# Kernel tuning notes

Hardware: AMD Instinct MI355X
Metric: run time of the kernel (lower is better)

Reference implementation:

```python
import jax, jax.numpy as jnp
import numpy as np

B, WAY, SHOT = 100, 5, 5            # B = way*shot + n_query = 25 + 75
C1, C2, D = 512, 640, 5             # F_L channels, F1 channels, disturb_num
S_L, S1 = 21, 42                    # F_L spatial, F1 spatial (square)
N = C2 * D                          # MLP width = 3200
WEIGHT = 0.5
EPS = 1e-5
GN_GROUPS = 16


def _dwconv1d(x, w):
    # x: (B, C, L), w: (C, 1, 7) depthwise, pad 3, no bias
    return jax.lax.conv_general_dilated(
        x, w, window_strides=(1,), padding=[(3, 3)],
        dimension_numbers=('NCH', 'OIH', 'NCH'),
        feature_group_count=x.shape[1])


def _group_norm(x, gamma, beta):
    # x: (B, C, L); GroupNorm(16, C), eps=1e-5
    b, c, l = x.shape
    xg = x.reshape(b, GN_GROUPS, -1)
    m = xg.mean(-1, keepdims=True)
    v = xg.var(-1, keepdims=True)
    xn = ((xg - m) * jax.lax.rsqrt(v + EPS)).reshape(b, c, l)
    return xn * gamma[None, :, None] + beta[None, :, None]


def setup_inputs() -> dict:
    key = jax.random.key(0)
    ks = jax.random.split(key, 8)
    inp = {
        'F1': jax.random.normal(ks[0], (B, C2, S1, S1), jnp.float32),
        'F_L': jax.random.normal(ks[1], (B, C1, S_L, S_L), jnp.float32),
        # structure_capture: depthwise Conv1d(C1, C1, 7, groups=C1, bias=False) + GroupNorm(16, C1)
        'sc_w': jax.random.normal(ks[2], (C1, 1, 7), jnp.float32) * 0.05,
        'gn_g': jnp.ones((C1,), jnp.float32),
        'gn_b': jnp.zeros((C1,), jnp.float32),
        # mask_branch: Conv2d(C1,16,1)+BN2d(16)+ReLU+Conv2d(16,D,1)
        'mb1_w': jax.random.normal(ks[3], (16, C1), jnp.float32) * 0.02,
        'mb1_b': jnp.zeros((16,), jnp.float32),
        'bn_g': jnp.ones((16,), jnp.float32),
        'bn_b': jnp.zeros((16,), jnp.float32),
        'mb2_w': jax.random.normal(ks[4], (D, 16), jnp.float32) * 0.02,
        'mb2_b': jnp.zeros((D,), jnp.float32),
        # both_mlp1 (resnet=True): BN1d(N) + Linear(N, N) + ELU
        'bn1d_g': jnp.ones((N,), jnp.float32),
        'bn1d_b': jnp.zeros((N,), jnp.float32),
        'lin_w': jax.random.normal(ks[5], (N, N), jnp.float32) * 0.01,
        'lin_b': jnp.zeros((N,), jnp.float32),
        'way': WAY,
        'shot': SHOT,
    }
    return inp


def _forward(F1, F_L, sc_w, gn_g, gn_b, mb1_w, mb1_b, bn_g, bn_b,
             mb2_w, mb2_b, bn1d_g, bn1d_b, lin_w, lin_b, way, shot):
    b = F_L.shape[0]
    # ---- structure_capture ----
    def gate(z):  # z: (B, C1, L)
        return jax.nn.sigmoid(_group_norm(_dwconv1d(z, sc_w), gn_g, gn_b))
    x_h = gate(F_L.mean(axis=3))[:, :, :, None]   # (B,C1,H,1)
    x_w = gate(F_L.mean(axis=2))[:, :, None, :]   # (B,C1,1,W)
    FLs = F_L * x_h * x_w

    # ---- bilinear upsample to F1 spatial (align_corners=False) ----
    s1 = F1.shape[-1]
    hm = jax.image.resize(FLs, (b, FLs.shape[1], s1, s1), method='bilinear')

    # ---- mask_branch (BatchNorm in eval mode: running_mean=0, running_var=1) ----
    h = jnp.einsum('bchw,oc->bohw', hm, mb1_w) + mb1_b[None, :, None, None]
    h = h * (bn_g * jax.lax.rsqrt(jnp.asarray(1.0 + EPS, h.dtype)))[None, :, None, None] \
        + bn_b[None, :, None, None]
    h = jax.nn.relu(h)
    heat = jnp.einsum('bchw,oc->bohw', h, mb2_w) + mb2_b[None, :, None, None]
    mask = jax.nn.sigmoid(heat)                   # (B, D, S1, S1)

    # ---- integration: fused weighted pooling (avoids (B,C2,D,HW) intermediate) ----
    f1 = F1.reshape(b, F1.shape[1], -1)           # (B, C2, HW)
    mk = mask.reshape(b, mask.shape[1], -1)       # (B, D, HW)
    sow = mk.sum(-1) + 1e-5                       # (B, D)
    vec = jnp.einsum('bcp,bdp->bcd', f1, mk) / sow[:, None, :]
    vec = vec.reshape(b, -1)                      # (B, C2*D)

    # ---- both_mlp1 (BN1d eval) + residual mix ----
    inv = jax.lax.rsqrt(jnp.asarray(1.0 + EPS, vec.dtype))
    z = vec * (bn1d_g * inv)[None, :] + bn1d_b[None, :]
    z = jax.nn.elu(z @ lin_w.T + lin_b[None, :])
    out = (1.0 - WEIGHT) * z + WEIGHT * vec

    support = out[:way * shot].reshape(way, shot, -1).mean(1)
    query = out[way * shot:]
    return support, query


def reference(F1, F_L, sc_w, gn_g, gn_b, mb1_w, mb1_b, bn_g, bn_b,
              mb2_w, mb2_b, bn1d_g, bn1d_b, lin_w, lin_b, way, shot):
    return _forward(F1, F_L, sc_w, gn_g, gn_b, mb1_w, mb1_b, bn_g, bn_b,
                    mb2_w, mb2_b, bn1d_g, bn1d_b, lin_w, lin_b, way, shot)
```

## Files before the change

kernel.cpp:

```cpp
#include <hip/hip_runtime.h>
#include <cstddef>

#define TPB 256

__device__ __forceinline__ float sigmoidf_(float x) {
  return 1.0f / (1.0f + __expf(-x));
}

__device__ __forceinline__ void rzmap(int i, int& j0, int& j1, float& w0, float& w1) {
  if (i == 0)            { j0 = 0;  j1 = 0;  w0 = 1.0f;  w1 = 0.0f; }
  else if (i == 41)      { j0 = 20; j1 = 20; w0 = 1.0f;  w1 = 0.0f; }
  else if ((i & 1) == 0) { int k = i >> 1; j0 = k - 1; j1 = k;     w0 = 0.25f; w1 = 0.75f; }
  else                   { int k = i >> 1; j0 = k;     j1 = k + 1; w0 = 0.75f; w1 = 0.25f; }
}

__global__ __launch_bounds__(256) void k1_gate_proj(
    const float* __restrict__ FL, const float* __restrict__ scw,
    const float* __restrict__ gng, const float* __restrict__ gnb,
    const float* __restrict__ mb1w, float* __restrict__ plc_part) {
  const int g = blockIdx.x, b = blockIdx.y;
  const int tid = threadIdx.x;
  __shared__ __align__(16) float slab[32 * 441];
  __shared__ float rm[672], cm[672], ch[672], cw[672];
  __shared__ float red[16];

  const float* base = FL + ((size_t)b * 512 + g * 32) * 441;
  const float4* b4 = (const float4*)base;
  float4* sl4 = (float4*)slab;
  for (int i = tid; i < 3528; i += TPB) sl4[i] = b4[i];
  __syncthreads();

  for (int idx = tid; idx < 672; idx += TPB) {
    int c = idx / 21, l = idx - c * 21;
    const float* rowp = slab + c * 441 + l * 21;
    float sr = 0.0f;
    #pragma unroll
    for (int w = 0; w < 21; ++w) sr += rowp[w];
    rm[idx] = sr * (1.0f / 21.0f);
    const float* colp = slab + c * 441 + l;
    float sc = 0.0f;
    #pragma unroll
    for (int h = 0; h < 21; ++h) sc += colp[h * 21];
    cm[idx] = sc * (1.0f / 21.0f);
  }
  __syncthreads();

  for (int idx = tid; idx < 672; idx += TPB) {
    int c = idx / 21, l = idx - c * 21;
    const float* w7 = scw + (g * 32 + c) * 7;
    float ah = 0.0f, aw = 0.0f;
    #pragma unroll
    for (int t = 0; t < 7; ++t) {
      int ll = l + t - 3;
      if (ll >= 0 && ll < 21) {
        float wt = w7[t];
        ah += rm[c * 21 + ll] * wt;
        aw += cm[c * 21 + ll] * wt;
      }
    }
    ch[idx] = ah; cw[idx] = aw;
  }
  __syncthreads();

  float s1 = 0.0f, s2 = 0.0f, s3 = 0.0f, s4v = 0.0f;
  for (int idx = tid; idx < 672; idx += TPB) {
    float x = ch[idx], y = cw[idx];
    s1 += x; s2 += x * x; s3 += y; s4v += y * y;
  }
  #pragma unroll
  for (int off = 32; off; off >>= 1) {
    s1 += __shfl_down(s1, off); s2 += __shfl_down(s2, off);
    s3 += __shfl_down(s3, off); s4v += __shfl_down(s4v, off);
  }
  if ((tid & 63) == 0) {
    int wv = tid >> 6;
    red[wv * 4 + 0] = s1; red[wv * 4 + 1] = s2;
    red[wv * 4 + 2] = s3; red[wv * 4 + 3] = s4v;
  }
  __syncthreads();
  const float S1 = red[0] + red[4] + red[8] + red[12];
  const float S2 = red[1] + red[5] + red[9] + red[13];
  const float S3 = red[2] + red[6] + red[10] + red[14];
  const float S4 = red[3] + red[7] + red[11] + red[15];
  const float invn = 1.0f / 672.0f;
  const float mh = S1 * invn, vh = S2 * invn - mh * mh;
  const float mw = S3 * invn, vw = S4 * invn - mw * mw;
  const float ivh = rsqrtf(vh + 1e-5f), ivw = rsqrtf(vw + 1e-5f);

  for (int idx = tid; idx < 672; idx += TPB) {
    int c = idx / 21;
    float gamma = gng[g * 32 + c], beta = gnb[g * 32 + c];
    ch[idx] = sigmoidf_((ch[idx] - mh) * ivh * gamma + beta);
    cw[idx] = sigmoidf_((cw[idx] - mw) * ivw * gamma + beta);
  }
  __syncthreads();

  float* pp = plc_part + ((size_t)g * 100 + b) * 7056;
  for (int p = tid; p < 441; p += TPB) {
    int i = p / 21, j = p - i * 21;
    float acc[16];
    #pragma unroll
    for (int o = 0; o < 16; ++o) acc[o] = 0.0f;
    #pragma unroll 4
    for (int c = 0; c < 32; ++c) {
      float v = slab[c * 441 + p] * ch[c * 21 + i] * cw[c * 21 + j];
      const float* wc = mb1w + g * 32 + c;
      #pragma unroll
      for (int o = 0; o < 16; ++o) acc[o] += v * wc[o * 512];
    }
    #pragma unroll
    for (int o = 0; o < 16; ++o) pp[(size_t)o * 441 + p] = acc[o];
  }
}

__global__ __launch_bounds__(256) void k1c_red(
    const float* __restrict__ pp, float* __restrict__ plc) {
  int i = blockIdx.x * TPB + threadIdx.x;
  if (i >= 705600) return;
  float s = 0.0f;
  #pragma unroll
  for (int g = 0; g < 16; ++g) s += pp[(size_t)g * 705600 + i];
  plc[i] = s;
}

__global__ __launch_bounds__(256) void k2_mask(
    const float* __restrict__ plc, const float* __restrict__ mb1b,
    const float* __restrict__ bng, const float* __restrict__ bnb,
    const float* __restrict__ mb2w, const float* __restrict__ mb2b,
    float* __restrict__ mask, float* __restrict__ sow) {
  const int b = blockIdx.x;
  const int p = blockIdx.y * TPB + threadIdx.x;
  float macc[5] = {0, 0, 0, 0, 0};
  if (p < 1764) {
    int y = p / 42, x = p - y * 42;
    int jy0, jy1, jx0, jx1; float wy0, wy1, wx0, wx1;
    rzmap(y, jy0, jy1, wy0, wy1);
    rzmap(x, jx0, jx1, wx0, wx1);
    const float RSQ = rsqrtf(1.0f + 1e-5f);
    const float* pb = plc + (size_t)b * 16 * 441;
    float h[16];
    #pragma unroll
    for (int o = 0; o < 16; ++o) {
      const float* po = pb + o * 441;
      float hm = wy0 * (wx0 * po[jy0 * 21 + jx0] + wx1 * po[jy0 * 21 + jx1]) +
                 wy1 * (wx0 * po[jy1 * 21 + jx0] + wx1 * po[jy1 * 21 + jx1]);
      float t = (hm + mb1b[o]) * (bng[o] * RSQ) + bnb[o];
      h[o] = t > 0.0f ? t : 0.0f;
    }
    #pragma unroll
    for (int d = 0; d < 5; ++d) {
      float acc = mb2b[d];
      #pragma unroll
      for (int o = 0; o < 16; ++o) acc += mb2w[d * 16 + o] * h[o];
      float mv = sigmoidf_(acc);
      mask[((size_t)b * 5 + d) * 1764 + p] = mv;
      macc[d] = mv;
    }
  }
  #pragma unroll
  for (int off = 32; off; off >>= 1) {
    #pragma unroll
    for (int d = 0; d < 5; ++d) macc[d] += __shfl_down(macc[d], off);
  }
  if ((threadIdx.x & 63) == 0) {
    #pragma unroll
    for (int d = 0; d < 5; ++d) atomicAdd(&sow[b * 5 + d], macc[d]);
  }
}

__global__ __launch_bounds__(256) void k3_vec(
    const float* __restrict__ F1, const float* __restrict__ mask,
    const float* __restrict__ sow, const float* __restrict__ g1d,
    float* __restrict__ vec_pad, float* __restrict__ vec_r) {
  const int ct = blockIdx.x, b = blockIdx.y;
  const int wv = threadIdx.x >> 6, lane = threadIdx.x & 63;
  const int c0 = ct * 16 + wv * 4;
  const float4* f0 = (const float4*)(F1 + ((size_t)b * 640 + c0) * 1764);
  const float4* mk = (const float4*)(mask + (size_t)b * 8820);
  float a[4][5] = {};
  for (int q = lane; q < 441; q += 64) {
    float4 f[4];
    #pragma unroll
    for (int j = 0; j < 4; ++j) f[j] = f0[(size_t)j * 441 + q];
    #pragma unroll
    for (int d = 0; d < 5; ++d) {
      float4 m = mk[d * 441 + q];
      #pragma unroll
      for (int j = 0; j < 4; ++j)
        a[j][d] += f[j].x * m.x + f[j].y * m.y + f[j].z * m.z + f[j].w * m.w;
    }
  }
  #pragma unroll
  for (int off = 32; off; off >>= 1) {
    #pragma unroll
    for (int j = 0; j < 4; ++j)
      #pragma unroll
      for (int d = 0; d < 5; ++d)
        a[j][d] += __shfl_down(a[j][d], off);
  }
  if (lane == 0) {
    const float RSQ = rsqrtf(1.0f + 1e-5f);
    #pragma unroll
    for (int j = 0; j < 4; ++j) {
      #pragma unroll
      for (int d = 0; d < 5; ++d) {
        float inv = 1.0f / (sow[b * 5 + d] + 1e-5f);
        float val = a[j][d] * inv;
        int k = (c0 + j) * 5 + d;
        vec_r[(size_t)b * 3200 + k] = val;
        vec_pad[(size_t)b * 3200 + k] = val * (g1d[k] * RSQ);
      }
    }
  }
}

__global__ __launch_bounds__(512) void k4_gemm(
    const float* __restrict__ A, const float* __restrict__ b1d,
    const float* __restrict__ W, float* __restrict__ dacc) {
  const int n0 = blockIdx.x * 64, ks = blockIdx.z;
  const int tid = threadIdx.x;
  const int tx = tid & 15, ty = tid >> 4;
  const int lr = tid >> 3, lq = tid & 7;
  __shared__ float4 As[8 * 132];
  __shared__ float4 Ws[8 * 68];
  const float4* A4 = (const float4*)A;
  const float4* B4 = (const float4*)b1d;
  const float4* W4 = (const float4*)W;
  const int kbase = ks * 80;
  const int r1 = lr + 64;
  float acc[4][4] = {};
  for (int kk = 0; kk < 10; ++kk) {
    __syncthreads();
    const int col = kbase + kk * 8 + lq;
    As[lq * 132 + lr] = A4[(size_t)lr * 800 + col];
    float4 va1;
    if (r1 < 100)       va1 = A4[(size_t)r1 * 800 + col];
    else if (r1 == 100) va1 = B4[col];
    else                va1 = make_float4(0.f, 0.f, 0.f, 0.f);
    As[lq * 132 + r1] = va1;
    Ws[lq * 68 + lr] = W4[(size_t)(n0 + lr) * 800 + col];
    __syncthreads();
    #pragma unroll
    for (int kq = 0; kq < 8; ++kq) {
      float4 av[4], bv[4];
      #pragma unroll
      for (int r = 0; r < 4; ++r) av[r] = As[kq * 132 + ty + 32 * r];
      #pragma unroll
      for (int s = 0; s < 4; ++s) bv[s] = Ws[kq * 68 + tx + 16 * s];
      #pragma unroll
      for (int r = 0; r < 4; ++r)
        #pragma unroll
        for (int s = 0; s < 4; ++s)
          acc[r][s] += av[r].x * bv[s].x + av[r].y * bv[s].y +
                       av[r].z * bv[s].z + av[r].w * bv[s].w;
    }
  }
  float* dp = dacc + (size_t)ks * 409600;
  #pragma unroll
  for (int r = 0; r < 4; ++r) {
    const int m = ty + 32 * r;
    #pragma unroll
    for (int s = 0; s < 4; ++s)
      dp[(size_t)m * 3200 + n0 + tx + 16 * s] = acc[r][s];
  }
}

__global__ __launch_bounds__(256) void k4b_epi(
    const float* __restrict__ dacc, const float* __restrict__ linb,
    const float* __restrict__ vec_r, float* __restrict__ out) {
  int i = blockIdx.x * TPB + threadIdx.x;
  if (i >= 320000) return;
  int m = i / 3200, n = i - m * 3200;
  const size_t S = 409600;
  size_t o = (size_t)m * 3200 + n;
  size_t oc = (size_t)100 * 3200 + n;
  float d = 0.0f, c0 = 0.0f;
  #pragma unroll
  for (int t = 0; t < 10; ++t) { d += dacc[t * S + o]; c0 += dacc[t * S + oc]; }
  float dv = d + c0 + linb[n];
  float z = dv > 0.0f ? dv : expm1f(dv);
  float ov = 0.5f * z + 0.5f * vec_r[i];
  if (m < 25) atomicAdd(out + (size_t)(m / 5) * 3200 + n, 0.2f * ov);
  else        out[(size_t)(m - 20) * 3200 + n] = ov;
}

extern "C" void kernel_launch(void* const* d_in, const int* in_sizes, int n_in,
                              void* d_out, int out_size, void* d_ws, size_t ws_size,
                              hipStream_t stream) {
  const float* F1   = (const float*)d_in[0];
  const float* FL   = (const float*)d_in[1];
  const float* scw  = (const float*)d_in[2];
  const float* gng  = (const float*)d_in[3];
  const float* gnb  = (const float*)d_in[4];
  const float* mb1w = (const float*)d_in[5];
  const float* mb1b = (const float*)d_in[6];
  const float* bng  = (const float*)d_in[7];
  const float* bnb  = (const float*)d_in[8];
  const float* mb2w = (const float*)d_in[9];
  const float* mb2b = (const float*)d_in[10];
  const float* g1d  = (const float*)d_in[11];
  const float* b1d  = (const float*)d_in[12];
  const float* linw = (const float*)d_in[13];
  const float* linb = (const float*)d_in[14];

  float* ws       = (float*)d_ws;
  float* plc      = ws;
  float* plc_part = ws + 705600;
  float* sow      = ws + 11995200;
  float* mask     = ws + 11995712;
  float* vec_pad  = ws + 12877712;
  float* vec_r    = ws + 13197712;
  float* dacc     = ws + 13517712;
  float* out      = (float*)d_out;

  hipMemsetAsync(sow, 0, 512 * sizeof(float), stream);
  hipMemsetAsync(out, 0, 16000 * sizeof(float), stream);
  k1_gate_proj<<<dim3(16, 100), TPB, 0, stream>>>(FL, scw, gng, gnb, mb1w, plc_part);
  k1c_red<<<dim3(2757), TPB, 0, stream>>>(plc_part, plc);
  k2_mask<<<dim3(100, 7), TPB, 0, stream>>>(plc, mb1b, bng, bnb, mb2w, mb2b, mask, sow);
  k3_vec<<<dim3(40, 100), TPB, 0, stream>>>(F1, mask, sow, g1d, vec_pad, vec_r);
  k4_gemm<<<dim3(50, 1, 10), 512, 0, stream>>>(vec_pad, b1d, linw, dacc);
  k4b_epi<<<dim3(1250), TPB, 0, stream>>>(dacc, linb, vec_r, out);
}
```

Before: 840.9 us.

## Halve gate-proj partials, recompute mask sums in k3, fold memsets into gemm

New measurement: 827.4 us. About the same (-1.6%).

```diff
diff --git a/kernel.cpp b/kernel.cpp
--- a/kernel.cpp
+++ b/kernel.cpp
@@ -18,98 +18,116 @@
     const float* __restrict__ FL, const float* __restrict__ scw,
     const float* __restrict__ gng, const float* __restrict__ gnb,
     const float* __restrict__ mb1w, float* __restrict__ plc_part) {
-  const int g = blockIdx.x, b = blockIdx.y;
+  const int gp = blockIdx.x, b = blockIdx.y;
   const int tid = threadIdx.x;
   __shared__ __align__(16) float slab[32 * 441];
   __shared__ float rm[672], cm[672], ch[672], cw[672];
   __shared__ float red[16];
 
-  const float* base = FL + ((size_t)b * 512 + g * 32) * 441;
-  const float4* b4 = (const float4*)base;
-  float4* sl4 = (float4*)slab;
-  for (int i = tid; i < 3528; i += TPB) sl4[i] = b4[i];
-  __syncthreads();
-
-  for (int idx = tid; idx < 672; idx += TPB) {
-    int c = idx / 21, l = idx - c * 21;
-    const float* rowp = slab + c * 441 + l * 21;
-    float sr = 0.0f;
-    #pragma unroll
-    for (int w = 0; w < 21; ++w) sr += rowp[w];
-    rm[idx] = sr * (1.0f / 21.0f);
-    const float* colp = slab + c * 441 + l;
-    float sc = 0.0f;
-    #pragma unroll
-    for (int h = 0; h < 21; ++h) sc += colp[h * 21];
-    cm[idx] = sc * (1.0f / 21.0f);
-  }
-  __syncthreads();
-
-  for (int idx = tid; idx < 672; idx += TPB) {
-    int c = idx / 21, l = idx - c * 21;
-    const float* w7 = scw + (g * 32 + c) * 7;
-    float ah = 0.0f, aw = 0.0f;
-    #pragma unroll
-    for (int t = 0; t < 7; ++t) {
-      int ll = l + t - 3;
-      if (ll >= 0 && ll < 21) {
-        float wt = w7[t];
-        ah += rm[c * 21 + ll] * wt;
-        aw += cm[c * 21 + ll] * wt;
+  const int p0 = tid;
+  const int p1 = tid + 256;
+  const int i0 = p0 / 21, j0 = p0 - i0 * 21;
+  const int i1 = p1 / 21, j1 = p1 - i1 * 21;
+  float acc0[16] = {}, acc1[16] = {};
+
+  for (int gi = 0; gi < 2; ++gi) {
+    const int g = gp * 2 + gi;
+    __syncthreads();
+
+    const float4* b4 = (const float4*)(FL + ((size_t)b * 512 + g * 32) * 441);
+    float4* sl4 = (float4*)slab;
+    for (int i = tid; i < 3528; i += TPB) sl4[i] = b4[i];
+    __syncthreads();
+
+    for (int idx = tid; idx < 672; idx += TPB) {
+      int c = idx / 21, l = idx - c * 21;
+      const float* rowp = slab + c * 441 + l * 21;
+      float sr = 0.0f;
+      #pragma unroll
+      for (int w = 0; w < 21; ++w) sr += rowp[w];
+      rm[idx] = sr * (1.0f / 21.0f);
+      const float* colp = slab + c * 441 + l;
+      float sc = 0.0f;
+      #pragma unroll
+      for (int h = 0; h < 21; ++h) sc += colp[h * 21];
+      cm[idx] = sc * (1.0f / 21.0f);
+    }
+    __syncthreads();
+
+    for (int idx = tid; idx < 672; idx += TPB) {
+      int c = idx / 21, l = idx - c * 21;
+      const float* w7 = scw + (g * 32 + c) * 7;
+      float ah = 0.0f, aw = 0.0f;
+      #pragma unroll
+      for (int t = 0; t < 7; ++t) {
+        int ll = l + t - 3;
+        if (ll >= 0 && ll < 21) {
+          float wt = w7[t];
+          ah += rm[c * 21 + ll] * wt;
+          aw += cm[c * 21 + ll] * wt;
+        }
       }
-    }
-    ch[idx] = ah; cw[idx] = aw;
-  }
-  __syncthreads();
-
-  float s1 = 0.0f, s2 = 0.0f, s3 = 0.0f, s4v = 0.0f;
-  for (int idx = tid; idx < 672; idx += TPB) {
-    float x = ch[idx], y = cw[idx];
-    s1 += x; s2 += x * x; s3 += y; s4v += y * y;
-  }
-  #pragma unroll
-  for (int off = 32; off; off >>= 1) {
-    s1 += __shfl_down(s1, off); s2 += __shfl_down(s2, off);
-    s3 += __shfl_down(s3, off); s4v += __shfl_down(s4v, off);
-  }
-  if ((tid & 63) == 0) {
-    int wv = tid >> 6;
-    red[wv * 4 + 0] = s1; red[wv * 4 + 1] = s2;
-    red[wv * 4 + 2] = s3; red[wv * 4 + 3] = s4v;
-  }
-  __syncthreads();
-  const float S1 = red[0] + red[4] + red[8] + red[12];
-  const float S2 = red[1] + red[5] + red[9] + red[13];
-  const float S3 = red[2] + red[6] + red[10] + red[14];
-  const float S4 = red[3] + red[7] + red[11] + red[15];
-  const float invn = 1.0f / 672.0f;
-  const float mh = S1 * invn, vh = S2 * invn - mh * mh;
-  const float mw = S3 * invn, vw = S4 * invn - mw * mw;
-  const float ivh = rsqrtf(vh + 1e-5f), ivw = rsqrtf(vw + 1e-5f);
-
-  for (int idx = tid; idx < 672; idx += TPB) {
-    int c = idx / 21;
-    float gamma = gng[g * 32 + c], beta = gnb[g * 32 + c];
-    ch[idx] = sigmoidf_((ch[idx] - mh) * ivh * gamma + beta);
-    cw[idx] = sigmoidf_((cw[idx] - mw) * ivw * gamma + beta);
-  }
-  __syncthreads();
-
-  float* pp = plc_part + ((size_t)g * 100 + b) * 7056;
-  for (int p = tid; p < 441; p += TPB) {
-    int i = p / 21, j = p - i * 21;
-    float acc[16];
-    #pragma unroll
-    for (int o = 0; o < 16; ++o) acc[o] = 0.0f;
+      ch[idx] = ah; cw[idx] = aw;
+    }
+    __syncthreads();
+
+    float s1 = 0.0f, s2 = 0.0f, s3 = 0.0f, s4v = 0.0f;
+    for (int idx = tid; idx < 672; idx += TPB) {
+      float x = ch[idx], y = cw[idx];
+      s1 += x; s2 += x * x; s3 += y; s4v += y * y;
+    }
+    #pragma unroll
+    for (int off = 32; off; off >>= 1) {
+      s1 += __shfl_down(s1, off); s2 += __shfl_down(s2, off);
+      s3 += __shfl_down(s3, off); s4v += __shfl_down(s4v, off);
+    }
+    if ((tid & 63) == 0) {
+      int wv = tid >> 6;
+      red[wv * 4 + 0] = s1; red[wv * 4 + 1] = s2;
+      red[wv * 4 + 2] = s3; red[wv * 4 + 3] = s4v;
+    }
+    __syncthreads();
+    const float S1 = red[0] + red[4] + red[8] + red[12];
+    const float S2 = red[1] + red[5] + red[9] + red[13];
+    const float S3 = red[2] + red[6] + red[10] + red[14];
+    const float S4 = red[3] + red[7] + red[11] + red[15];
+    const float invn = 1.0f / 672.0f;
+    const float mh = S1 * invn, vh = S2 * invn - mh * mh;
+    const float mw = S3 * invn, vw = S4 * invn - mw * mw;
+    const float ivh = rsqrtf(vh + 1e-5f), ivw = rsqrtf(vw + 1e-5f);
+
+    for (int idx = tid; idx < 672; idx += TPB) {
+      int c = idx / 21;
+      float gamma = gng[g * 32 + c], beta = gnb[g * 32 + c];
+      ch[idx] = sigmoidf_((ch[idx] - mh) * ivh * gamma + beta);
+      cw[idx] = sigmoidf_((cw[idx] - mw) * ivw * gamma + beta);
+    }
+    __syncthreads();
+
     #pragma unroll 4
     for (int c = 0; c < 32; ++c) {
-      float v = slab[c * 441 + p] * ch[c * 21 + i] * cw[c * 21 + j];
+      float v = slab[c * 441 + p0] * ch[c * 21 + i0] * cw[c * 21 + j0];
       const float* wc = mb1w + g * 32 + c;
       #pragma unroll
-      for (int o = 0; o < 16; ++o) acc[o] += v * wc[o * 512];
-    }
-    #pragma unroll
-    for (int o = 0; o < 16; ++o) pp[(size_t)o * 441 + p] = acc[o];
+      for (int o = 0; o < 16; ++o) acc0[o] += v * wc[o * 512];
+    }
+    if (p1 < 441) {
+      #pragma unroll 4
+      for (int c = 0; c < 32; ++c) {
+        float v = slab[c * 441 + p1] * ch[c * 21 + i1] * cw[c * 21 + j1];
+        const float* wc = mb1w + g * 32 + c;
+        #pragma unroll
+        for (int o = 0; o < 16; ++o) acc1[o] += v * wc[o * 512];
+      }
+    }
+  }
+
+  float* pp = plc_part + ((size_t)gp * 100 + b) * 7056;
+  #pragma unroll
+  for (int o = 0; o < 16; ++o) pp[(size_t)o * 441 + p0] = acc0[o];
+  if (p1 < 441) {
+    #pragma unroll
+    for (int o = 0; o < 16; ++o) pp[(size_t)o * 441 + p1] = acc1[o];
   }
 }
 
@@ -119,7 +137,7 @@
   if (i >= 705600) return;
   float s = 0.0f;
   #pragma unroll
-  for (int g = 0; g < 16; ++g) s += pp[(size_t)g * 705600 + i];
+  for (int g = 0; g < 8; ++g) s += pp[(size_t)g * 705600 + i];
   plc[i] = s;
 }
 
@@ -127,50 +145,37 @@
     const float* __restrict__ plc, const float* __restrict__ mb1b,
     const float* __restrict__ bng, const float* __restrict__ bnb,
     const float* __restrict__ mb2w, const float* __restrict__ mb2b,
-    float* __restrict__ mask, float* __restrict__ sow) {
+    float* __restrict__ mask) {
   const int b = blockIdx.x;
   const int p = blockIdx.y * TPB + threadIdx.x;
-  float macc[5] = {0, 0, 0, 0, 0};
-  if (p < 1764) {
-    int y = p / 42, x = p - y * 42;
-    int jy0, jy1, jx0, jx1; float wy0, wy1, wx0, wx1;
-    rzmap(y, jy0, jy1, wy0, wy1);
-    rzmap(x, jx0, jx1, wx0, wx1);
-    const float RSQ = rsqrtf(1.0f + 1e-5f);
-    const float* pb = plc + (size_t)b * 16 * 441;
-    float h[16];
-    #pragma unroll
-    for (int o = 0; o < 16; ++o) {
-      const float* po = pb + o * 441;
-      float hm = wy0 * (wx0 * po[jy0 * 21 + jx0] + wx1 * po[jy0 * 21 + jx1]) +
-                 wy1 * (wx0 * po[jy1 * 21 + jx0] + wx1 * po[jy1 * 21 + jx1]);
-      float t = (hm + mb1b[o]) * (bng[o] * RSQ) + bnb[o];
-      h[o] = t > 0.0f ? t : 0.0f;
-    }
-    #pragma unroll
-    for (int d = 0; d < 5; ++d) {
-      float acc = mb2b[d];
-      #pragma unroll
-      for (int o = 0; o < 16; ++o) acc += mb2w[d * 16 + o] * h[o];
-      float mv = sigmoidf_(acc);
-      mask[((size_t)b * 5 + d) * 1764 + p] = mv;
-      macc[d] = mv;
-    }
-  }
-  #pragma unroll
-  for (int off = 32; off; off >>= 1) {
-    #pragma unroll
-    for (int d = 0; d < 5; ++d) macc[d] += __shfl_down(macc[d], off);
-  }
-  if ((threadIdx.x & 63) == 0) {
-    #pragma unroll
-    for (int d = 0; d < 5; ++d) atomicAdd(&sow[b * 5 + d], macc[d]);
+  if (p >= 1764) return;
+  int y = p / 42, x = p - y * 42;
+  int jy0, jy1, jx0, jx1; float wy0, wy1, wx0, wx1;
+  rzmap(y, jy0, jy1, wy0, wy1);
+  rzmap(x, jx0, jx1, wx0, wx1);
+  const float RSQ = rsqrtf(1.0f + 1e-5f);
+  const float* pb = plc + (size_t)b * 16 * 441;
+  float h[16];
+  #pragma unroll
+  for (int o = 0; o < 16; ++o) {
+    const float* po = pb + o * 441;
+    float hm = wy0 * (wx0 * po[jy0 * 21 + jx0] + wx1 * po[jy0 * 21 + jx1]) +
+               wy1 * (wx0 * po[jy1 * 21 + jx0] + wx1 * po[jy1 * 21 + jx1]);
+    float t = (hm + mb1b[o]) * (bng[o] * RSQ) + bnb[o];
+    h[o] = t > 0.0f ? t : 0.0f;
+  }
+  #pragma unroll
+  for (int d = 0; d < 5; ++d) {
+    float acc = mb2b[d];
+    #pragma unroll
+    for (int o = 0; o < 16; ++o) acc += mb2w[d * 16 + o] * h[o];
+    mask[((size_t)b * 5 + d) * 1764 + p] = sigmoidf_(acc);
   }
 }
 
 __global__ __launch_bounds__(256) void k3_vec(
     const float* __restrict__ F1, const float* __restrict__ mask,
-    const float* __restrict__ sow, const float* __restrict__ g1d,
+    const float* __restrict__ g1d,
     float* __restrict__ vec_pad, float* __restrict__ vec_r) {
   const int ct = blockIdx.x, b = blockIdx.y;
   const int wv = threadIdx.x >> 6, lane = threadIdx.x & 63;
@@ -178,6 +183,7 @@
   const float4* f0 = (const float4*)(F1 + ((size_t)b * 640 + c0) * 1764);
   const float4* mk = (const float4*)(mask + (size_t)b * 8820);
   float a[4][5] = {};
+  float sw[5] = {};
   for (int q = lane; q < 441; q += 64) {
     float4 f[4];
     #pragma unroll
@@ -185,6 +191,7 @@
     #pragma unroll
     for (int d = 0; d < 5; ++d) {
       float4 m = mk[d * 441 + q];
+      sw[d] += m.x + m.y + m.z + m.w;
       #pragma unroll
       for (int j = 0; j < 4; ++j)
         a[j][d] += f[j].x * m.x + f[j].y * m.y + f[j].z * m.z + f[j].w * m.w;
@@ -193,19 +200,22 @@
   #pragma unroll
   for (int off = 32; off; off >>= 1) {
     #pragma unroll
-    for (int j = 0; j < 4; ++j)
-      #pragma unroll
-      for (int d = 0; d < 5; ++d)
-        a[j][d] += __shfl_down(a[j][d], off);
+    for (int d = 0; d < 5; ++d) {
+      sw[d] += __shfl_down(sw[d], off);
+      #pragma unroll
+      for (int j = 0; j < 4; ++j) a[j][d] += __shfl_down(a[j][d], off);
+    }
   }
   if (lane == 0) {
     const float RSQ = rsqrtf(1.0f + 1e-5f);
+    float inv[5];
+    #pragma unroll
+    for (int d = 0; d < 5; ++d) inv[d] = 1.0f / (sw[d] + 1e-5f);
     #pragma unroll
     for (int j = 0; j < 4; ++j) {
       #pragma unroll
       for (int d = 0; d < 5; ++d) {
-        float inv = 1.0f / (sow[b * 5 + d] + 1e-5f);
-        float val = a[j][d] * inv;
+        float val = a[j][d] * inv[d];
         int k = (c0 + j) * 5 + d;
         vec_r[(size_t)b * 3200 + k] = val;
         vec_pad[(size_t)b * 3200 + k] = val * (g1d[k] * RSQ);
@@ -216,13 +226,18 @@
 
 __global__ __launch_bounds__(512) void k4_gemm(
     const float* __restrict__ A, const float* __restrict__ b1d,
-    const float* __restrict__ W, float* __restrict__ dacc) {
+    const float* __restrict__ W, float* __restrict__ dacc,
+    float* __restrict__ outz) {
   const int n0 = blockIdx.x * 64, ks = blockIdx.z;
   const int tid = threadIdx.x;
   const int tx = tid & 15, ty = tid >> 4;
   const int lr = tid >> 3, lq = tid & 7;
   __shared__ float4 As[8 * 132];
   __shared__ float4 Ws[8 * 68];
+  if (ks == 0) {
+    int zi = blockIdx.x * 512 + tid;
+    if (zi < 16000) outz[zi] = 0.0f;
+  }
   const float4* A4 = (const float4*)A;
   const float4* B4 = (const float4*)b1d;
   const float4* W4 = (const float4*)W;
@@ -306,19 +321,16 @@
   float* ws       = (float*)d_ws;
   float* plc      = ws;
   float* plc_part = ws + 705600;
-  float* sow      = ws + 11995200;
-  float* mask     = ws + 11995712;
-  float* vec_pad  = ws + 12877712;
-  float* vec_r    = ws + 13197712;
-  float* dacc     = ws + 13517712;
+  float* mask     = ws + 6350400;
+  float* vec_pad  = ws + 7232400;
+  float* vec_r    = ws + 7552400;
+  float* dacc     = ws + 7872400;
   float* out      = (float*)d_out;
 
-  hipMemsetAsync(sow, 0, 512 * sizeof(float), stream);
-  hipMemsetAsync(out, 0, 16000 * sizeof(float), stream);
-  k1_gate_proj<<<dim3(16, 100), TPB, 0, stream>>>(FL, scw, gng, gnb, mb1w, plc_part);
+  k1_gate_proj<<<dim3(8, 100), TPB, 0, stream>>>(FL, scw, gng, gnb, mb1w, plc_part);
   k1c_red<<<dim3(2757), TPB, 0, stream>>>(plc_part, plc);
-  k2_mask<<<dim3(100, 7), TPB, 0, stream>>>(plc, mb1b, bng, bnb, mb2w, mb2b, mask, sow);
-  k3_vec<<<dim3(40, 100), TPB, 0, stream>>>(F1, mask, sow, g1d, vec_pad, vec_r);
-  k4_gemm<<<dim3(50, 1, 10), 512, 0, stream>>>(vec_pad, b1d, linw, dacc);
+  k2_mask<<<dim3(100, 7), TPB, 0, stream>>>(plc, mb1b, bng, bnb, mb2w, mb2b, mask);
+  k3_vec<<<dim3(40, 100), TPB, 0, stream>>>(F1, mask, g1d, vec_pad, vec_r);
+  k4_gemm<<<dim3(50, 1, 10), 512, 0, stream>>>(vec_pad, b1d, linw, dacc, out);
   k4b_epi<<<dim3(1250), TPB, 0, stream>>>(dacc, linb, vec_r, out);
 }
```
